# Kernel optimization log

Hardware: AMD Instinct MI355X
Metric: run time of the kernel (lower is better)

The kernel has to match this reference:

```python
import jax, jax.numpy as jnp
import numpy as np

DIM = 768
HEADS = 8
HEAD_DIM = DIM // HEADS
SCALE = HEAD_DIM ** -0.5
EPS = 1e-5


def layernorm(x, gamma, beta):
    mu = jnp.mean(x, axis=-1, keepdims=True)
    var = jnp.mean((x - mu) ** 2, axis=-1, keepdims=True)
    return (x - mu) * jax.lax.rsqrt(var + EPS) * gamma + beta


def setup_inputs() -> dict:
    key = jax.random.key(0)
    ks = jax.random.split(key, 12)
    B, L, M, D = 8, 1024, 1024, DIM
    s = D ** -0.5
    return {
        "x": jax.random.normal(ks[0], (B, L, D), jnp.float32),
        "context": jax.random.normal(ks[1], (B, M, D), jnp.float32),
        "Wq": jax.random.normal(ks[2], (D, D), jnp.float32) * s,
        "bq": jnp.zeros((D,), jnp.float32),
        "Wkv": jax.random.normal(ks[3], (D, 2 * D), jnp.float32) * s,
        "bkv": jnp.zeros((2 * D,), jnp.float32),
        "Wp": jax.random.normal(ks[4], (D, D), jnp.float32) * s,
        "bp": jnp.zeros((D,), jnp.float32),
        "g1": jnp.ones((D,), jnp.float32),
        "b1": jnp.zeros((D,), jnp.float32),
        "g2": jnp.ones((D,), jnp.float32),
        "b2": jnp.zeros((D,), jnp.float32),
    }


def reference(x, context, Wq, bq, Wkv, bkv, Wp, bp, g1, b1, g2, b2):
    B, L, D = x.shape
    M = context.shape[1]
    Hp = Wp_ = int(L ** 0.5)
    x_n = layernorm(x, g1, b1)
    c_n = layernorm(context, g2, b2)
    q = (x_n @ Wq + bq).reshape(B, L, HEADS, HEAD_DIM).transpose(0, 2, 1, 3)  # bhld
    kv = (c_n @ Wkv + bkv).reshape(B, M, 2, HEADS, HEAD_DIM).transpose(2, 0, 3, 1, 4)
    k, v = kv[0], kv[1]  # bhmd
    attn = jnp.einsum("bhld,bhmd->bhlm", q, k) * SCALE
    w = jax.nn.softmax(attn, axis=-1)
    attn_map = w.mean(axis=1).sum(axis=-1).reshape(B, Hp, Wp_)
    out = jnp.einsum("bhlm,bhmd->bhld", w, v).transpose(0, 2, 1, 3).reshape(B, L, D)
    out = out @ Wp + bp
    # dropout is identity in eval mode (training=False)
    return out + x, attn_map
```

## Files before the change

kernel.cpp:

```cpp
#include <hip/hip_runtime.h>

typedef unsigned short u16;
typedef short bf16x8 __attribute__((ext_vector_type(8)));
typedef float f32x4 __attribute__((ext_vector_type(4)));
typedef unsigned short u16x8 __attribute__((ext_vector_type(8)));
typedef unsigned short u16x4 __attribute__((ext_vector_type(4)));

union bfr { unsigned int u[4]; bf16x8 v; };

__device__ __forceinline__ u16 f2bf(float f) {
    unsigned int u = __builtin_bit_cast(unsigned int, f);
    u = (u + 0x7fffu + ((u >> 16) & 1u)) >> 16;
    return (u16)u;
}

__device__ __forceinline__ unsigned int cvtpk(float lo, float hi) {
    unsigned int r;
    asm("v_cvt_pk_bf16_f32 %0, %1, %2" : "=v"(r) : "v"(lo), "v"(hi));
    return r;
}

__device__ __forceinline__ void gload16(const u16* src, u16* lds_dst) {
    __builtin_amdgcn_global_load_lds(
        (const __attribute__((address_space(1))) unsigned int*)src,
        (__attribute__((address_space(3))) unsigned int*)lds_dst, 16, 0, 0);
}

__global__ __launch_bounds__(256) void prep_ln_k(
    const float* __restrict__ x, const float* __restrict__ ctx,
    const float* __restrict__ g1, const float* __restrict__ b1,
    const float* __restrict__ g2, const float* __restrict__ b2,
    const float* __restrict__ Wq, const float* __restrict__ Wkv,
    const float* __restrict__ Wp,
    u16* __restrict__ xn, u16* __restrict__ cn,
    u16* __restrict__ WqT, u16* __restrict__ WkvT, u16* __restrict__ WpT)
{
    const int id = blockIdx.x;
    const int t = threadIdx.x;
    if (id >= 16384) {
        __shared__ float T[64][65];
        int t2 = id - 16384;
        const float* src; u16* dst; int lds, k0, n0;
        if (t2 < 288) { src = Wkv; dst = WkvT; lds = 1536; k0 = (t2 / 24) * 64; n0 = (t2 % 24) * 64; }
        else if (t2 < 432) { int u = t2 - 288; src = Wq; dst = WqT; lds = 768; k0 = (u / 12) * 64; n0 = (u % 12) * 64; }
        else { int u = t2 - 432; src = Wp; dst = WpT; lds = 768; k0 = (u / 12) * 64; n0 = (u % 12) * 64; }
        const int rr = t >> 4, c4 = (t & 15) * 4;
        #pragma unroll
        for (int it = 0; it < 4; it++) {
            int r = rr + it * 16;
            f32x4 v = *(const f32x4*)&src[(long)(k0 + r) * lds + n0 + c4];
            #pragma unroll
            for (int j = 0; j < 4; j++) T[c4 + j][r] = v[j];
        }
        __syncthreads();
        #pragma unroll
        for (int it = 0; it < 4; it++) {
            int r = rr + it * 16;
            u16x4 w;
            #pragma unroll
            for (int j = 0; j < 4; j++) w[j] = f2bf(T[r][c4 + j]);
            *(u16x4*)&dst[(long)(n0 + r) * 768 + k0 + c4] = w;
        }
        return;
    }
    const float* src; const float* g; const float* b; u16* dst;
    if (id < 8192) { src = x + (long)id * 768; g = g1; b = b1; dst = xn + (long)id * 768; }
    else { int r = id - 8192; src = ctx + (long)r * 768; g = g2; b = b2; dst = cn + (long)r * 768; }

    int lane = t & 63, wid = t >> 6;
    float v0 = src[t], v1 = src[t + 256], v2 = src[t + 512];
    float s = v0 + v1 + v2;
    for (int o = 32; o; o >>= 1) s += __shfl_xor(s, o);
    __shared__ float r1[4], r2[4];
    if (!lane) r1[wid] = s;
    __syncthreads();
    float mu = (r1[0] + r1[1] + r1[2] + r1[3]) * (1.0f / 768.0f);
    float d0 = v0 - mu, d1 = v1 - mu, d2 = v2 - mu;
    float q = d0 * d0 + d1 * d1 + d2 * d2;
    for (int o = 32; o; o >>= 1) q += __shfl_xor(q, o);
    if (!lane) r2[wid] = q;
    __syncthreads();
    float var = (r2[0] + r2[1] + r2[2] + r2[3]) * (1.0f / 768.0f);
    float rs = rsqrtf(var + 1e-5f);
    dst[t]       = f2bf(d0 * rs * g[t]       + b[t]);
    dst[t + 256] = f2bf(d1 * rs * g[t + 256] + b[t + 256]);
    dst[t + 512] = f2bf(d2 * rs * g[t + 512] + b[t + 512]);
}

__global__ __launch_bounds__(256) void qkv_k(
    const u16* __restrict__ xn, const u16* __restrict__ cn,
    const u16* __restrict__ WqT, const u16* __restrict__ WkvT,
    const float* __restrict__ bq, const float* __restrict__ bkv,
    u16* __restrict__ Qb, u16* __restrict__ Kb, u16* __restrict__ Vt)
{
    __shared__ u16 As[128 * 32];
    __shared__ u16 Bs[128 * 32];
    const int id = blockIdx.x;
    const int swz = (id & 7) * 144 + (id >> 3);
    const int tid = threadIdx.x, lane = tid & 63, wid = tid >> 6;
    const int wr = wid >> 1, wc = wid & 1;
    const int g = lane >> 4, i15 = lane & 15;

    const bool isQ = swz < 384;
    int rt, ct;
    const u16* A; const u16* Bt; const float* bias;
    if (isQ) { rt = swz / 6;  ct = swz % 6;  A = xn; Bt = WqT;  bias = bq; }
    else { int s2 = swz - 384; rt = s2 / 12; ct = s2 % 12; A = cn; Bt = WkvT; bias = bkv; }
    const int row0 = rt * 128, col0 = ct * 128;

    const u16* srcA[2]; const u16* srcB[2]; int ldsOff[2];
    #pragma unroll
    for (int c = 0; c < 2; c++) {
        int P0 = (wid * 2 + c) * 1024;
        int P = P0 + lane * 16;
        int r = P >> 6;
        int slot = (P >> 4) & 3;
        int colx = ((slot ^ ((r >> 1) & 3)) << 3);
        srcA[c] = A  + (long)(row0 + r) * 768 + colx;
        srcB[c] = Bt + (long)(col0 + r) * 768 + colx;
        ldsOff[c] = P0 >> 1;
    }

    int aoff[4], boff[4];
    #pragma unroll
    for (int m = 0; m < 4; m++) {
        int R = wr * 64 + m * 16 + i15;
        aoff[m] = R * 32 + ((g ^ ((R >> 1) & 3)) << 3);
    }
    #pragma unroll
    for (int n = 0; n < 4; n++) {
        int R = wc * 64 + n * 16 + i15;
        boff[n] = R * 32 + ((g ^ ((R >> 1) & 3)) << 3);
    }

    f32x4 acc[4][4] = {};
    for (int k0 = 0; k0 < 768; k0 += 32) {
        __syncthreads();
        #pragma unroll
        for (int c = 0; c < 2; c++) {
            gload16(srcA[c] + k0, &As[ldsOff[c]]);
            gload16(srcB[c] + k0, &Bs[ldsOff[c]]);
        }
        __syncthreads();
        bf16x8 av[4], bv[4];
        #pragma unroll
        for (int m = 0; m < 4; m++) av[m] = *(const bf16x8*)&As[aoff[m]];
        #pragma unroll
        for (int n = 0; n < 4; n++) bv[n] = *(const bf16x8*)&Bs[boff[n]];
        #pragma unroll
        for (int m = 0; m < 4; m++)
            #pragma unroll
            for (int n = 0; n < 4; n++)
                acc[m][n] = __builtin_amdgcn_mfma_f32_16x16x32_bf16(av[m], bv[n], acc[m][n], 0, 0, 0);
    }

    float bv4[4];
    #pragma unroll
    for (int n = 0; n < 4; n++) bv4[n] = bias[col0 + wc * 64 + n * 16 + i15];

    #pragma unroll
    for (int m = 0; m < 4; m++) {
        #pragma unroll
        for (int n = 0; n < 4; n++) {
            const int col = col0 + wc * 64 + n * 16 + i15;
            #pragma unroll
            for (int r = 0; r < 4; r++) {
                const int row = row0 + wr * 64 + m * 16 + g * 4 + r;
                float v = acc[m][n][r];
                if (isQ) {
                    v = (v + bv4[n]) * 0.14724444706f;
                    int b = row >> 10, l = row & 1023;
                    int h = col / 96, d = col % 96;
                    Qb[((long)(b * 8 + h) * 1024 + l) * 96 + d] = f2bf(v);
                } else {
                    v += bv4[n];
                    int b = row >> 10, mt = row & 1023;
                    if (col < 768) {
                        int h = col / 96, d = col % 96;
                        Kb[((long)(b * 8 + h) * 1024 + mt) * 96 + d] = f2bf(v);
                    } else {
                        int cc = col - 768;
                        int h = cc / 96, d = cc % 96;
                        Vt[((long)(b * 8 + h) * 96 + d) * 1024 + mt] = f2bf(v);
                    }
                }
            }
        }
    }
}

__global__ __launch_bounds__(256) void flash_k(
    const u16* __restrict__ Qb, const u16* __restrict__ Kb,
    const u16* __restrict__ Vt, u16* __restrict__ Ob)
{
    const int i = blockIdx.x;
    const int s8 = i >> 3;
    const int bh = (i & 7) * 8 + (s8 >> 4);
    const int qt = s8 & 15;
    const int tid = threadIdx.x, lane = tid & 63, wid = tid >> 6;
    const int g = lane >> 4, i15 = lane & 15;

    __shared__ u16 Ks[2][6144];
    __shared__ u16 Vs[2][6144];

    const long baseQK = (long)bh * 98304;
    const u16* Kt  = Kb + baseQK;
    const u16* Vtp = Vt + baseQK;

    bf16x8 qf[3];
    {
        const u16* qrow = Qb + baseQK + (long)(qt * 64 + wid * 16 + i15) * 96 + g * 8;
        qf[0] = *(const bf16x8*)(qrow);
        qf[1] = *(const bf16x8*)(qrow + 32);
        qf[2] = *(const bf16x8*)(qrow + 64);
    }

    int krd[4][3];
    #pragma unroll
    for (int n = 0; n < 4; n++) {
        int q4 = i15 >> 2, rr = i15 & 3, m = n >> 1;
        int R = (n & 1) ? (m * 32 + ((q4 ^ 2) << 3) + 4 + rr)
                        : (m * 32 + (q4 << 3) + rr);
        #pragma unroll
        for (int kd = 0; kd < 3; kd++)
            krd[n][kd] = kd * 2048 + R * 32 + ((g ^ ((R >> 3) & 3) ^ kd) << 3);
    }
    int vrd[6][2];
    #pragma unroll
    for (int n6 = 0; n6 < 6; n6++) {
        int row = n6 * 16 + i15;
        #pragma unroll
        for (int kk = 0; kk < 2; kk++)
            vrd[n6][kk] = row * 64 + ((kk * 32 + g * 8) ^ ((row & 7) << 3));
    }

    int kgo[3], kwr[3], vgo[3], vwr[3];
    #pragma unroll
    for (int it = 0; it < 3; it++) {
        int e = tid + it * 256;
        int r = e / 12, cEl = (e % 12) * 8;
        int kd = cEl >> 5, slot = (cEl >> 3) & 3;
        kgo[it] = r * 96 + cEl;
        kwr[it] = kd * 2048 + r * 32 + ((slot ^ ((r >> 3) & 3) ^ kd) << 3);
        int d = e >> 3, m8 = (e & 7) * 8;
        vgo[it] = d * 1024 + m8;
        vwr[it] = d * 64 + (m8 ^ ((d & 7) << 3));
    }

    u16x8 kreg[3], vreg[3];
    #pragma unroll
    for (int it = 0; it < 3; it++) {
        kreg[it] = *(const u16x8*)&Kt[kgo[it]];
        vreg[it] = *(const u16x8*)&Vtp[vgo[it]];
    }
    #pragma unroll
    for (int it = 0; it < 3; it++) {
        *(u16x8*)&Ks[0][kwr[it]] = kreg[it];
        *(u16x8*)&Vs[0][vwr[it]] = vreg[it];
    }

    f32x4 o[6] = {};
    float lsum = 0.f;
    int cur = 0;

    for (int t = 0; t < 16; t++) {
        __syncthreads();
        if (t < 15) {
            #pragma unroll
            for (int it = 0; it < 3; it++) {
                kreg[it] = *(const u16x8*)&Kt[(t + 1) * 6144 + kgo[it]];
                vreg[it] = *(const u16x8*)&Vtp[(t + 1) * 64 + vgo[it]];
            }
        }

        f32x4 s[4] = {};
        #pragma unroll
        for (int kd = 0; kd < 3; kd++) {
            #pragma unroll
            for (int n = 0; n < 4; n++) {
                bf16x8 kf = *(const bf16x8*)&Ks[cur][krd[n][kd]];
                s[n] = __builtin_amdgcn_mfma_f32_16x16x32_bf16(kf, qf[kd], s[n], 0, 0, 0);
            }
        }

        unsigned int pk[4][2];
        #pragma unroll
        for (int n = 0; n < 4; n++) {
            float p0 = exp2f(s[n][0]), p1 = exp2f(s[n][1]);
            float p2 = exp2f(s[n][2]), p3 = exp2f(s[n][3]);
            lsum += (p0 + p1) + (p2 + p3);
            pk[n][0] = cvtpk(p0, p1);
            pk[n][1] = cvtpk(p2, p3);
        }

        #pragma unroll
        for (int kk = 0; kk < 2; kk++) {
            bfr pa;
            pa.u[0] = pk[kk * 2][0];
            pa.u[1] = pk[kk * 2][1];
            pa.u[2] = __shfl_xor(pk[kk * 2 + 1][0], 32);
            pa.u[3] = __shfl_xor(pk[kk * 2 + 1][1], 32);
            #pragma unroll
            for (int n6 = 0; n6 < 6; n6++) {
                bf16x8 vf = *(const bf16x8*)&Vs[cur][vrd[n6][kk]];
                o[n6] = __builtin_amdgcn_mfma_f32_16x16x32_bf16(pa.v, vf, o[n6], 0, 0, 0);
            }
        }

        if (t < 15) {
            #pragma unroll
            for (int it = 0; it < 3; it++) {
                *(u16x8*)&Ks[cur ^ 1][kwr[it]] = kreg[it];
                *(u16x8*)&Vs[cur ^ 1][vwr[it]] = vreg[it];
            }
        }
        cur ^= 1;
    }

    lsum += __shfl_xor(lsum, 16);
    lsum += __shfl_xor(lsum, 32);
    float linv = 1.0f / lsum;

    const int b = bh >> 3, h = bh & 7;
    #pragma unroll
    for (int r = 0; r < 4; r++) {
        float lr = __shfl(linv, g * 4 + r);
        int row = qt * 64 + wid * 16 + g * 4 + r;
        long base = ((long)(b * 1024 + row)) * 768 + h * 96;
        #pragma unroll
        for (int n6 = 0; n6 < 6; n6++)
            Ob[base + n6 * 16 + i15] = f2bf(o[n6][r] * lr);
    }
}

__global__ __launch_bounds__(256) void out_k(
    const u16* __restrict__ Ob, const u16* __restrict__ WpT,
    const float* __restrict__ bp, const float* __restrict__ resid,
    float* __restrict__ out, float* __restrict__ amap)
{
    const int id = blockIdx.x;
    if (id >= 384) {
        amap[(id - 384) * 256 + threadIdx.x] = 1.0f;
        return;
    }
    __shared__ u16 As[128 * 32];
    __shared__ u16 Bs[128 * 32];
    const int swz = (id & 7) * 48 + (id >> 3);
    const int rt = swz / 6, ct = swz % 6;
    const int row0 = rt * 128, col0 = ct * 128;
    const int tid = threadIdx.x, lane = tid & 63, wid = tid >> 6;
    const int wr = wid >> 1, wc = wid & 1;
    const int g = lane >> 4, i15 = lane & 15;

    const u16* srcA[2]; const u16* srcB[2]; int ldsOff[2];
    #pragma unroll
    for (int c = 0; c < 2; c++) {
        int P0 = (wid * 2 + c) * 1024;
        int P = P0 + lane * 16;
        int r = P >> 6;
        int slot = (P >> 4) & 3;
        int colx = ((slot ^ ((r >> 1) & 3)) << 3);
        srcA[c] = Ob  + (long)(row0 + r) * 768 + colx;
        srcB[c] = WpT + (long)(col0 + r) * 768 + colx;
        ldsOff[c] = P0 >> 1;
    }

    int aoff[4], boff[4];
    #pragma unroll
    for (int m = 0; m < 4; m++) {
        int R = wr * 64 + m * 16 + i15;
        aoff[m] = R * 32 + ((g ^ ((R >> 1) & 3)) << 3);
    }
    #pragma unroll
    for (int n = 0; n < 4; n++) {
        int R = wc * 64 + n * 16 + i15;
        boff[n] = R * 32 + ((g ^ ((R >> 1) & 3)) << 3);
    }

    f32x4 acc[4][4] = {};
    for (int k0 = 0; k0 < 768; k0 += 32) {
        __syncthreads();
        #pragma unroll
        for (int c = 0; c < 2; c++) {
            gload16(srcA[c] + k0, &As[ldsOff[c]]);
            gload16(srcB[c] + k0, &Bs[ldsOff[c]]);
        }
        __syncthreads();
        bf16x8 av[4], bv[4];
        #pragma unroll
        for (int m = 0; m < 4; m++) av[m] = *(const bf16x8*)&As[aoff[m]];
        #pragma unroll
        for (int n = 0; n < 4; n++) bv[n] = *(const bf16x8*)&Bs[boff[n]];
        #pragma unroll
        for (int m = 0; m < 4; m++)
            #pragma unroll
            for (int n = 0; n < 4; n++)
                acc[m][n] = __builtin_amdgcn_mfma_f32_16x16x32_bf16(av[m], bv[n], acc[m][n], 0, 0, 0);
    }

    float bv4[4];
    #pragma unroll
    for (int n = 0; n < 4; n++) bv4[n] = bp[col0 + wc * 64 + n * 16 + i15];

    #pragma unroll
    for (int m = 0; m < 4; m++) {
        #pragma unroll
        for (int n = 0; n < 4; n++) {
            const int col = col0 + wc * 64 + n * 16 + i15;
            #pragma unroll
            for (int r = 0; r < 4; r++) {
                const int row = row0 + wr * 64 + m * 16 + g * 4 + r;
                long idx = (long)row * 768 + col;
                out[idx] = acc[m][n][r] + bv4[n] + resid[idx];
            }
        }
    }
}

extern "C" void kernel_launch(void* const* d_in, const int* in_sizes, int n_in,
                              void* d_out, int out_size, void* d_ws, size_t ws_size,
                              hipStream_t stream)
{
    const float* x   = (const float*)d_in[0];
    const float* ctx = (const float*)d_in[1];
    const float* Wq  = (const float*)d_in[2];
    const float* bq  = (const float*)d_in[3];
    const float* Wkv = (const float*)d_in[4];
    const float* bkv = (const float*)d_in[5];
    const float* Wp  = (const float*)d_in[6];
    const float* bp  = (const float*)d_in[7];
    const float* g1  = (const float*)d_in[8];
    const float* b1  = (const float*)d_in[9];
    const float* g2  = (const float*)d_in[10];
    const float* b2  = (const float*)d_in[11];
    float* out = (float*)d_out;

    char* w = (char*)d_ws;
    const long SZ_ROWS = 8192L * 768 * 2;
    long off = 0;
    u16* xn   = (u16*)(w + off); off += SZ_ROWS;
    u16* cn   = (u16*)(w + off); off += SZ_ROWS;
    u16* WqT  = (u16*)(w + off); off += 768L * 768 * 2;
    u16* WkvT = (u16*)(w + off); off += 1536L * 768 * 2;
    u16* WpT  = (u16*)(w + off); off += 768L * 768 * 2;
    u16* Qb   = (u16*)(w + off); off += SZ_ROWS;
    u16* Kb   = (u16*)(w + off); off += SZ_ROWS;
    u16* Vt   = (u16*)(w + off); off += SZ_ROWS;
    u16* Ob   = (u16*)(w + off); off += SZ_ROWS;

    prep_ln_k<<<16960, 256, 0, stream>>>(x, ctx, g1, b1, g2, b2, Wq, Wkv, Wp,
                                         xn, cn, WqT, WkvT, WpT);
    qkv_k<<<1152, 256, 0, stream>>>(xn, cn, WqT, WkvT, bq, bkv, Qb, Kb, Vt);
    flash_k<<<1024, 256, 0, stream>>>(Qb, Kb, Vt, Ob);
    out_k<<<416, 256, 0, stream>>>(Ob, WpT, bp, x, out, out + 6291456L);
}
```

Baseline: 158.0 us.

## Use wave-per-row LayerNorm, stagger QKV K-loop start, single-buffer K tile

The LayerNorm prep now gives each wavefront one row and uses vectorized float4 loads and stores. Block reductions become wave shuffles with no shared memory or barriers, and the grid shrinks to 4672 blocks. The QKV GEMM rotates each block's starting K offset so concurrent blocks read different columns, which should spread memory channel and cache traffic. Flash attention single-buffers the K tile and adds an extra barrier mid-iteration, saving LDS for occupancy at the cost of one more sync per step.

```diff
diff --git a/kernel.cpp b/kernel.cpp
--- a/kernel.cpp
+++ b/kernel.cpp
@@ -37,9 +37,9 @@
 {
     const int id = blockIdx.x;
     const int t = threadIdx.x;
-    if (id >= 16384) {
+    if (id >= 4096) {
         __shared__ float T[64][65];
-        int t2 = id - 16384;
+        int t2 = id - 4096;
         const float* src; u16* dst; int lds, k0, n0;
         if (t2 < 288) { src = Wkv; dst = WkvT; lds = 1536; k0 = (t2 / 24) * 64; n0 = (t2 % 24) * 64; }
         else if (t2 < 432) { int u = t2 - 288; src = Wq; dst = WqT; lds = 768; k0 = (u / 12) * 64; n0 = (u % 12) * 64; }
@@ -63,28 +63,45 @@
         }
         return;
     }
+    const int lane = t & 63, w = t >> 6;
+    const int row = id * 4 + w;
     const float* src; const float* g; const float* b; u16* dst;
-    if (id < 8192) { src = x + (long)id * 768; g = g1; b = b1; dst = xn + (long)id * 768; }
-    else { int r = id - 8192; src = ctx + (long)r * 768; g = g2; b = b2; dst = cn + (long)r * 768; }
-
-    int lane = t & 63, wid = t >> 6;
-    float v0 = src[t], v1 = src[t + 256], v2 = src[t + 512];
-    float s = v0 + v1 + v2;
+    if (row < 8192) { src = x + (long)row * 768; g = g1; b = b1; dst = xn + (long)row * 768; }
+    else { int r = row - 8192; src = ctx + (long)r * 768; g = g2; b = b2; dst = cn + (long)r * 768; }
+
+    const int c0 = lane * 4;
+    f32x4 v0 = *(const f32x4*)&src[c0];
+    f32x4 v1 = *(const f32x4*)&src[c0 + 256];
+    f32x4 v2 = *(const f32x4*)&src[c0 + 512];
+    float s = (v0[0] + v0[1] + v0[2] + v0[3]) + (v1[0] + v1[1] + v1[2] + v1[3])
+            + (v2[0] + v2[1] + v2[2] + v2[3]);
+    #pragma unroll
     for (int o = 32; o; o >>= 1) s += __shfl_xor(s, o);
-    __shared__ float r1[4], r2[4];
-    if (!lane) r1[wid] = s;
-    __syncthreads();
-    float mu = (r1[0] + r1[1] + r1[2] + r1[3]) * (1.0f / 768.0f);
-    float d0 = v0 - mu, d1 = v1 - mu, d2 = v2 - mu;
-    float q = d0 * d0 + d1 * d1 + d2 * d2;
+    const float mu = s * (1.0f / 768.0f);
+    float q = 0.f;
+    #pragma unroll
+    for (int j = 0; j < 4; j++) { float d = v0[j] - mu; q += d * d; }
+    #pragma unroll
+    for (int j = 0; j < 4; j++) { float d = v1[j] - mu; q += d * d; }
+    #pragma unroll
+    for (int j = 0; j < 4; j++) { float d = v2[j] - mu; q += d * d; }
+    #pragma unroll
     for (int o = 32; o; o >>= 1) q += __shfl_xor(q, o);
-    if (!lane) r2[wid] = q;
-    __syncthreads();
-    float var = (r2[0] + r2[1] + r2[2] + r2[3]) * (1.0f / 768.0f);
-    float rs = rsqrtf(var + 1e-5f);
-    dst[t]       = f2bf(d0 * rs * g[t]       + b[t]);
-    dst[t + 256] = f2bf(d1 * rs * g[t + 256] + b[t + 256]);
-    dst[t + 512] = f2bf(d2 * rs * g[t + 512] + b[t + 512]);
+    const float rs = rsqrtf(q * (1.0f / 768.0f) + 1e-5f);
+
+    f32x4 ga0 = *(const f32x4*)&g[c0],       ba0 = *(const f32x4*)&b[c0];
+    f32x4 ga1 = *(const f32x4*)&g[c0 + 256], ba1 = *(const f32x4*)&b[c0 + 256];
+    f32x4 ga2 = *(const f32x4*)&g[c0 + 512], ba2 = *(const f32x4*)&b[c0 + 512];
+    u16x4 w0, w1, w2;
+    #pragma unroll
+    for (int j = 0; j < 4; j++) {
+        w0[j] = f2bf((v0[j] - mu) * rs * ga0[j] + ba0[j]);
+        w1[j] = f2bf((v1[j] - mu) * rs * ga1[j] + ba1[j]);
+        w2[j] = f2bf((v2[j] - mu) * rs * ga2[j] + ba2[j]);
+    }
+    *(u16x4*)&dst[c0]       = w0;
+    *(u16x4*)&dst[c0 + 256] = w1;
+    *(u16x4*)&dst[c0 + 512] = w2;
 }
 
 __global__ __launch_bounds__(256) void qkv_k(
@@ -134,12 +151,13 @@
     }
 
     f32x4 acc[4][4] = {};
-    for (int k0 = 0; k0 < 768; k0 += 32) {
+    int kc = ((id >> 3) % 24) * 32;
+    for (int t = 0; t < 24; t++) {
         __syncthreads();
         #pragma unroll
         for (int c = 0; c < 2; c++) {
-            gload16(srcA[c] + k0, &As[ldsOff[c]]);
-            gload16(srcB[c] + k0, &Bs[ldsOff[c]]);
+            gload16(srcA[c] + kc, &As[ldsOff[c]]);
+            gload16(srcB[c] + kc, &Bs[ldsOff[c]]);
         }
         __syncthreads();
         bf16x8 av[4], bv[4];
@@ -152,6 +170,8 @@
             #pragma unroll
             for (int n = 0; n < 4; n++)
                 acc[m][n] = __builtin_amdgcn_mfma_f32_16x16x32_bf16(av[m], bv[n], acc[m][n], 0, 0, 0);
+        kc += 32;
+        if (kc == 768) kc = 0;
     }
 
     float bv4[4];
@@ -200,7 +220,7 @@
     const int tid = threadIdx.x, lane = tid & 63, wid = tid >> 6;
     const int g = lane >> 4, i15 = lane & 15;
 
-    __shared__ u16 Ks[2][6144];
+    __shared__ u16 Ks[6144];
     __shared__ u16 Vs[2][6144];
 
     const long baseQK = (long)bh * 98304;
@@ -255,7 +275,7 @@
     }
     #pragma unroll
     for (int it = 0; it < 3; it++) {
-        *(u16x8*)&Ks[0][kwr[it]] = kreg[it];
+        *(u16x8*)&Ks[kwr[it]] = kreg[it];
         *(u16x8*)&Vs[0][vwr[it]] = vreg[it];
     }
 
@@ -278,9 +298,15 @@
         for (int kd = 0; kd < 3; kd++) {
             #pragma unroll
             for (int n = 0; n < 4; n++) {
-                bf16x8 kf = *(const bf16x8*)&Ks[cur][krd[n][kd]];
+                bf16x8 kf = *(const bf16x8*)&Ks[krd[n][kd]];
                 s[n] = __builtin_amdgcn_mfma_f32_16x16x32_bf16(kf, qf[kd], s[n], 0, 0, 0);
             }
+        }
+        __syncthreads();
+        if (t < 15) {
+            #pragma unroll
+            for (int it = 0; it < 3; it++)
+                *(u16x8*)&Ks[kwr[it]] = kreg[it];
         }
 
         unsigned int pk[4][2];
@@ -309,10 +335,8 @@
 
         if (t < 15) {
             #pragma unroll
-            for (int it = 0; it < 3; it++) {
-                *(u16x8*)&Ks[cur ^ 1][kwr[it]] = kreg[it];
+            for (int it = 0; it < 3; it++)
                 *(u16x8*)&Vs[cur ^ 1][vwr[it]] = vreg[it];
-            }
         }
         cur ^= 1;
     }
@@ -448,8 +472,8 @@
     u16* Vt   = (u16*)(w + off); off += SZ_ROWS;
     u16* Ob   = (u16*)(w + off); off += SZ_ROWS;
 
-    prep_ln_k<<<16960, 256, 0, stream>>>(x, ctx, g1, b1, g2, b2, Wq, Wkv, Wp,
-                                         xn, cn, WqT, WkvT, WpT);
+    prep_ln_k<<<4672, 256, 0, stream>>>(x, ctx, g1, b1, g2, b2, Wq, Wkv, Wp,
+                                        xn, cn, WqT, WkvT, WpT);
     qkv_k<<<1152, 256, 0, stream>>>(xn, cn, WqT, WkvT, bq, bkv, Qb, Kb, Vt);
     flash_k<<<1024, 256, 0, stream>>>(Qb, Kb, Vt, Ob);
     out_k<<<416, 256, 0, stream>>>(Ob, WpT, bp, x, out, out + 6291456L);
```

Result: faster. 154.7 us (-2.1%).
